# Kernel tuning notes

Hardware: AMD Instinct MI355X
Metric: run time of the kernel (lower is better)

## Reference

```python
import jax, jax.numpy as jnp
import numpy as np

D, H, HD, L, F, V, R, C = 512, 8, 64, 12, 2048, 2048, 1024, 64
B, T, M = 8, 1024, 128


def posenc(t, d):
    pos = jnp.arange(t, dtype=jnp.float32)[:, None]
    div = jnp.exp(jnp.arange(0, d, 2, dtype=jnp.float32) * (-np.log(10000.0) / d))
    pe = jnp.zeros((t, d), jnp.float32)
    pe = pe.at[:, 0::2].set(jnp.sin(pos * div))
    pe = pe.at[:, 1::2].set(jnp.cos(pos * div))
    return pe


def setup_inputs():
    key = jax.random.key(0)
    ks = iter(jax.random.split(key, 32))
    s = 0.02
    x = jax.random.randint(next(ks), (B, T), 1, V)  # avoid padding_idx=0 rows
    chord_positions = jax.random.randint(next(ks), (B, M), 0, T)
    n = lambda shape: jax.random.normal(next(ks), shape, jnp.float32) * s
    emb = n((V, D)).at[0].set(0.0)  # padding_idx row zeroed
    return {
        'x': x, 'chord_positions': chord_positions, 'emb': emb,
        'rel_emb': n((L, 2 * R + 1, HD)),
        'Wq': n((L, D, D)), 'bq': jnp.zeros((L, D)),
        'Wk': n((L, D, D)), 'bk': jnp.zeros((L, D)),
        'Wv': n((L, D, D)), 'bv': jnp.zeros((L, D)),
        'Wo': n((L, D, D)), 'bo': jnp.zeros((L, D)),
        'ln1_s': jnp.ones((L, D)), 'ln1_b': jnp.zeros((L, D)),
        'W1': n((L, D, F)), 'b1': jnp.zeros((L, F)),
        'W2': n((L, F, D)), 'b2': jnp.zeros((L, D)),
        'ln2_s': jnp.ones((L, D)), 'ln2_b': jnp.zeros((L, D)),
        'Wout': n((D, V)), 'bout': jnp.zeros((V,)),
        'Wc': n((D, C)), 'bc': jnp.zeros((C,)),
    }


def _ln(z, s, b):
    mu = jnp.mean(z, -1, keepdims=True)
    var = jnp.var(z, -1, keepdims=True)
    return (z - mu) * jax.lax.rsqrt(var + 1e-5) * s + b


def _forward(x, chord_positions, emb, rel_emb, Wq, bq, Wk, bk, Wv, bv, Wo, bo,
             ln1_s, ln1_b, W1, b1, W2, b2, ln2_s, ln2_b, Wout, bout, Wc, bc):
    Bx, Tx = x.shape
    h = emb[x] * jnp.sqrt(jnp.float32(D)) + posenc(Tx, D)[None]
    pad = (x == 0)  # key padding mask
    causal = jnp.triu(jnp.ones((Tx, Tx), bool), 1)
    mask = causal[None, None] | pad[:, None, None, :]  # (B,1|H,T,T)
    rel_idx = jnp.clip(jnp.arange(Tx)[None, :] - jnp.arange(Tx)[:, None], -R, R) + R  # (T,T)
    for i in range(L):
        q = (h @ Wq[i] + bq[i]).reshape(Bx, Tx, H, HD).transpose(0, 2, 1, 3)
        k = (h @ Wk[i] + bk[i]).reshape(Bx, Tx, H, HD).transpose(0, 2, 1, 3)
        v = (h @ Wv[i] + bv[i]).reshape(Bx, Tx, H, HD).transpose(0, 2, 1, 3)
        scores = jnp.einsum('bhqd,bhkd->bhqk', q, k)
        relp = jnp.einsum('bhqd,rd->bhqr', q, rel_emb[i])  # (B,H,T,2R+1)
        scores = scores + jnp.take_along_axis(relp, rel_idx[None, None], axis=-1)
        scores = scores * (1.0 / np.sqrt(HD))
        scores = jnp.where(mask, -1e9, scores)
        a = jax.nn.softmax(scores, axis=-1)
        o = jnp.einsum('bhqk,bhkd->bhqd', a, v).transpose(0, 2, 1, 3).reshape(Bx, Tx, D)
        h = _ln(h + o @ Wo[i] + bo[i], ln1_s[i], ln1_b[i])
        f = jax.nn.relu(h @ W1[i] + b1[i]) @ W2[i] + b2[i]
        h = _ln(h + f, ln2_s[i], ln2_b[i])
    logits = h @ Wout + bout
    safe_pos = jnp.maximum(chord_positions, 0)
    gathered = h[jnp.arange(Bx)[:, None], safe_pos]  # (B,M,D)
    chord_logits = gathered @ Wc + bc
    return logits, chord_logits


def reference(x, chord_positions, emb, rel_emb, Wq, bq, Wk, bk, Wv, bv, Wo, bo,
              ln1_s, ln1_b, W1, b1, W2, b2, ln2_s, ln2_b, Wout, bout, Wc, bc):
    return _forward(x, chord_positions, emb, rel_emb, Wq, bq, Wk, bk, Wv, bv, Wo, bo,
                    ln1_s, ln1_b, W1, b1, W2, b2, ln2_s, ln2_b, Wout, bout, Wc, bc)
```

## Files before the change

### kernel.cpp

```cpp
#include <hip/hip_runtime.h>
#include <hip/hip_bf16.h>
#include <cstddef>

constexpr int B_ = 8, TT = 1024, H_ = 8, HD_ = 64, D_ = 512, F_ = 2048;
constexpr int L_ = 12, R_ = 1024, NR_ = 2049, C_ = 64, M_ = 128, V_ = 2048;
constexpr int BT_ = B_ * TT;

typedef short bf16x8_t __attribute__((ext_vector_type(8)));
typedef float f32x4_t __attribute__((ext_vector_type(4)));
typedef unsigned short ushort_t;

__device__ __forceinline__ float b2f(unsigned int u16) {
  return __uint_as_float(u16 << 16);
}
__device__ __forceinline__ ushort_t f2b(float f) {
  __hip_bfloat16 h = __float2bfloat16(f);
  return *reinterpret_cast<ushort_t*>(&h);
}

__global__ __launch_bounds__(256) void transpose_bf16_b(const float* __restrict__ src,
                                                        ushort_t* __restrict__ dst,
                                                        int K, int N,
                                                        size_t sstride, size_t dstride) {
  __shared__ float t[32][33];
  src += (size_t)blockIdx.z * sstride;
  dst += (size_t)blockIdx.z * dstride;
  int k0 = blockIdx.y * 32, n0 = blockIdx.x * 32;
  int r = threadIdx.x >> 3, c4 = (threadIdx.x & 7) * 4;
  float4 vv = *(const float4*)(src + (size_t)(k0 + r) * N + n0 + c4);
  t[r][c4] = vv.x; t[r][c4 + 1] = vv.y; t[r][c4 + 2] = vv.z; t[r][c4 + 3] = vv.w;
  __syncthreads();
  ushort4 w;
  w.x = f2b(t[c4 + 0][r]); w.y = f2b(t[c4 + 1][r]);
  w.z = f2b(t[c4 + 2][r]); w.w = f2b(t[c4 + 3][r]);
  *(ushort4*)(dst + (size_t)(n0 + r) * K + k0 + c4) = w;
}

__global__ __launch_bounds__(256) void rel_convert(const float* __restrict__ rel,
                                                   ushort_t* __restrict__ rel_bf) {
  size_t idx = ((size_t)blockIdx.x * 256 + threadIdx.x) * 4;
  const size_t total = (size_t)L_ * NR_ * HD_;
  if (idx >= total) return;
  float4 f = *(const float4*)(rel + idx);
  ushort4 w;
  w.x = f2b(f.x); w.y = f2b(f.y); w.z = f2b(f.z); w.w = f2b(f.w);
  *(ushort4*)(rel_bf + idx) = w;
}

__global__ __launch_bounds__(256) void pack_bias(const float* __restrict__ bq,
                                                 const float* __restrict__ bk,
                                                 const float* __restrict__ bv,
                                                 float* __restrict__ bqkv) {
  int idx = blockIdx.x * 256 + threadIdx.x;
  if (idx >= L_ * 1536) return;
  int l = idx / 1536, c = idx - l * 1536;
  float v;
  if (c < 512) v = bq[l * 512 + c];
  else if (c < 1024) v = bk[l * 512 + (c - 512)];
  else v = bv[l * 512 + (c - 1024)];
  bqkv[idx] = v;
}

__global__ __launch_bounds__(256) void posenc_kernel(float* __restrict__ pe) {
  int t = blockIdx.x;
  int i = threadIdx.x;
  const float c = -9.210340371976184f / 512.0f;
  float div = expf((float)(2 * i) * c);
  float arg = (float)t * div;
  float sv, cv;
  __sincosf(arg, &sv, &cv);
  *(float2*)&pe[(size_t)t * D_ + 2 * i] = make_float2(sv, cv);
}

__global__ __launch_bounds__(256) void embed_kernel(const int* __restrict__ x,
                                                    const float* __restrict__ emb,
                                                    const float* __restrict__ pe,
                                                    float* __restrict__ h,
                                                    ushort_t* __restrict__ h_bf) {
  int bt = blockIdx.x;
  int t = bt & (TT - 1);
  int tok = x[bt];
  size_t base = (size_t)bt * D_;
  size_t ebase = (size_t)tok * D_;
  int d = threadIdx.x * 2;
  float2 e2 = *(const float2*)&emb[ebase + d];
  float2 p2 = *(const float2*)&pe[(size_t)t * D_ + d];
  float v0 = e2.x * 22.627416997969522f + p2.x;
  float v1 = e2.y * 22.627416997969522f + p2.y;
  *(float2*)&h[base + d] = make_float2(v0, v1);
  unsigned int ob = (unsigned int)f2b(v0) | ((unsigned int)f2b(v1) << 16);
  *(unsigned int*)&h_bf[base + d] = ob;
}

template <int OUT_BF16, int RELU>
__global__ __launch_bounds__(256) void gemm_mfma(const ushort_t* __restrict__ A,
                                                 const ushort_t* __restrict__ Bt,
                                                 const float* __restrict__ bias,
                                                 void* __restrict__ Cout,
                                                 int Mm, int N, int K) {
  __shared__ ushort_t As[128 * 32];
  __shared__ ushort_t Bs[128 * 32];
  int tid = threadIdx.x;
  int m0 = blockIdx.y * 128, n0 = blockIdx.x * 128;
  int lane = tid & 63, wid = tid >> 6;
  int wr = wid >> 1, wc = wid & 1;

  f32x4_t acc[4][4];
#pragma unroll
  for (int mi = 0; mi < 4; ++mi)
#pragma unroll
    for (int ni = 0; ni < 4; ++ni) acc[mi][ni] = (f32x4_t){0.f, 0.f, 0.f, 0.f};

  int c0 = tid, c1 = tid + 256;
  int ar0 = c0 >> 2, ap0 = c0 & 3, akg0 = ap0 ^ ((ar0 >> 1) & 3);
  int ar1 = c1 >> 2, ap1 = c1 & 3, akg1 = ap1 ^ ((ar1 >> 1) & 3);
  const ushort_t* Arow0 = A + (size_t)(m0 + ar0) * K + akg0 * 8;
  const ushort_t* Arow1 = A + (size_t)(m0 + ar1) * K + akg1 * 8;
  const ushort_t* Brow0 = Bt + (size_t)(n0 + ar0) * K + akg0 * 8;
  const ushort_t* Brow1 = Bt + (size_t)(n0 + ar1) * K + akg1 * 8;

  uint4 ra0 = *(const uint4*)(Arow0);
  uint4 ra1 = *(const uint4*)(Arow1);
  uint4 rb0 = *(const uint4*)(Brow0);
  uint4 rb1 = *(const uint4*)(Brow1);

  int NT = K >> 5;
  int kg = lane >> 4, rl = lane & 15;
  for (int kt = 0; kt < NT; ++kt) {
    __syncthreads();
    *(uint4*)&As[ar0 * 32 + ap0 * 8] = ra0;
    *(uint4*)&As[ar1 * 32 + ap1 * 8] = ra1;
    *(uint4*)&Bs[ar0 * 32 + ap0 * 8] = rb0;
    *(uint4*)&Bs[ar1 * 32 + ap1 * 8] = rb1;
    __syncthreads();
    if (kt + 1 < NT) {
      int ko = (kt + 1) << 5;
      ra0 = *(const uint4*)(Arow0 + ko);
      ra1 = *(const uint4*)(Arow1 + ko);
      rb0 = *(const uint4*)(Brow0 + ko);
      rb1 = *(const uint4*)(Brow1 + ko);
    }
    bf16x8_t fa[4], fb[4];
#pragma unroll
    for (int mi = 0; mi < 4; ++mi) {
      int r = wr * 64 + mi * 16 + rl;
      fa[mi] = *(bf16x8_t*)&As[r * 32 + ((kg ^ ((r >> 1) & 3)) << 3)];
    }
#pragma unroll
    for (int ni = 0; ni < 4; ++ni) {
      int r = wc * 64 + ni * 16 + rl;
      fb[ni] = *(bf16x8_t*)&Bs[r * 32 + ((kg ^ ((r >> 1) & 3)) << 3)];
    }
#pragma unroll
    for (int mi = 0; mi < 4; ++mi)
#pragma unroll
      for (int ni = 0; ni < 4; ++ni)
        acc[mi][ni] = __builtin_amdgcn_mfma_f32_16x16x32_bf16(fa[mi], fb[ni], acc[mi][ni], 0, 0, 0);
  }

  int rg = lane >> 4;
#pragma unroll
  for (int ni = 0; ni < 4; ++ni) {
    int col = n0 + wc * 64 + ni * 16 + rl;
    float bv = bias[col];
#pragma unroll
    for (int mi = 0; mi < 4; ++mi) {
      int row0 = m0 + wr * 64 + mi * 16 + rg * 4;
#pragma unroll
      for (int r = 0; r < 4; ++r) {
        float vv = acc[mi][ni][r] + bv;
        if (RELU) vv = fmaxf(vv, 0.0f);
        if (OUT_BF16)
          ((ushort_t*)Cout)[(size_t)(row0 + r) * N + col] = f2b(vv);
        else
          ((float*)Cout)[(size_t)(row0 + r) * N + col] = vv;
      }
    }
  }
}

__global__ __launch_bounds__(256) void chord_mfma(const ushort_t* __restrict__ h_bf,
                                                  const int* __restrict__ pos,
                                                  const ushort_t* __restrict__ wcT,
                                                  const float* __restrict__ bc,
                                                  float* __restrict__ out) {
  __shared__ ushort_t As[64 * 32];
  __shared__ ushort_t Bs[64 * 32];
  int tid = threadIdx.x;
  int lane = tid & 63, w = tid >> 6;
  int rl = lane & 15, kg = lane >> 4;
  int m0 = blockIdx.x * 64;
  int ar = tid >> 2, ap = tid & 3, akg = ap ^ ((ar >> 1) & 3);
  int grow = m0 + ar;
  int b = grow >> 7;
  int p = pos[grow];
  if (p < 0) p = 0;
  const ushort_t* asrc = h_bf + ((size_t)(b * TT + p)) * D_ + akg * 8;
  const ushort_t* bsrc = wcT + (size_t)ar * D_ + akg * 8;

  f32x4_t acc[4];
#pragma unroll
  for (int ni = 0; ni < 4; ++ni) acc[ni] = (f32x4_t){0.f, 0.f, 0.f, 0.f};

  for (int kt = 0; kt < 16; ++kt) {
    uint4 va = *(const uint4*)(asrc + kt * 32);
    uint4 vb = *(const uint4*)(bsrc + kt * 32);
    __syncthreads();
    *(uint4*)&As[ar * 32 + ap * 8] = va;
    *(uint4*)&Bs[ar * 32 + ap * 8] = vb;
    __syncthreads();
    int r = 16 * w + rl;
    bf16x8_t fa = *(bf16x8_t*)&As[r * 32 + ((kg ^ ((r >> 1) & 3)) << 3)];
#pragma unroll
    for (int ni = 0; ni < 4; ++ni) {
      int rr = ni * 16 + rl;
      bf16x8_t fb = *(bf16x8_t*)&Bs[rr * 32 + ((kg ^ ((rr >> 1) & 3)) << 3)];
      acc[ni] = __builtin_amdgcn_mfma_f32_16x16x32_bf16(fa, fb, acc[ni], 0, 0, 0);
    }
  }

  int rg = lane >> 4;
#pragma unroll
  for (int ni = 0; ni < 4; ++ni) {
    int col = ni * 16 + rl;
    float bv = bc[col];
#pragma unroll
    for (int r = 0; r < 4; ++r) {
      int row = m0 + 16 * w + rg * 4 + r;
      out[(size_t)row * C_ + col] = acc[ni][r] + bv;
    }
  }
}

__global__ __launch_bounds__(256) void attn_mfma(const ushort_t* __restrict__ qkv,
                                                 const ushort_t* __restrict__ rel_bf,
                                                 ushort_t* __restrict__ o) {
  __shared__ ushort_t QPs[64 * 64];
  __shared__ ushort_t Ks[64 * 64];
  __shared__ ushort_t Vs[64 * 64];
  __shared__ ushort_t Rl[128 * 64];

  int blk = blockIdx.x;
  int u = ((blk & 15) + 5 * ((blk >> 8) & 3)) & 15;
  int qt = (u & 1) ? ((u - 1) >> 1) : (15 - (u >> 1));
  int bh = blk >> 4;
  int hh = bh & 7, b = bh >> 3;
  int t0 = qt << 6;
  int tid = threadIdx.x;
  int lane = tid & 63, w = tid >> 6;
  int lo = lane & 15, hi = lane >> 4;

  const ushort_t* qg = qkv + ((size_t)(b * TT + t0)) * 1536 + hh * 64;
  const ushort_t* kg = qkv + ((size_t)b * TT) * 1536 + 512 + hh * 64;
  const ushort_t* vg = qkv + ((size_t)b * TT) * 1536 + 1024 + hh * 64;
  const ushort_t* relb = rel_bf + (size_t)(961 - t0) * 64;

  int row_a = tid >> 3, gg_a = tid & 7;
  int row_b = row_a + 32;

  for (int idx = tid; idx < 512; idx += 256) {
    int row = idx >> 3, gg = idx & 7;
    uint4 uu = *(const uint4*)(qg + (size_t)row * 1536 + gg * 8);
    unsigned int uw[4] = {uu.x, uu.y, uu.z, uu.w};
    unsigned int ow[4];
#pragma unroll
    for (int j = 0; j < 4; ++j) {
      float f0 = b2f(uw[j] & 0xffffu) * 0.125f;
      float f1 = b2f(uw[j] >> 16) * 0.125f;
      ow[j] = (unsigned int)f2b(f0) | ((unsigned int)f2b(f1) << 16);
    }
    *(uint4*)&QPs[row * 64 + ((gg ^ (row & 7)) << 3)] = make_uint4(ow[0], ow[1], ow[2], ow[3]);
  }
  __syncthreads();

  bf16x8_t faq0 = *(bf16x8_t*)&QPs[(16 * w + lo) * 64 + ((hi ^ (lo & 7)) << 3)];
  bf16x8_t faq1 = *(bf16x8_t*)&QPs[(16 * w + lo) * 64 + (((hi + 4) ^ (lo & 7)) << 3)];

  uint4 pk0 = *(const uint4*)(kg + (size_t)row_a * 1536 + gg_a * 8);
  uint4 pk1 = *(const uint4*)(kg + (size_t)row_b * 1536 + gg_a * 8);
  uint4 pv0 = *(const uint4*)(vg + (size_t)row_a * 1536 + gg_a * 8);
  uint4 pv1 = *(const uint4*)(vg + (size_t)row_b * 1536 + gg_a * 8);
  uint4 pr0 = *(const uint4*)(relb + (size_t)row_a * 64 + gg_a * 8);
  uint4 pr1 = *(const uint4*)(relb + (size_t)(row_a + 32) * 64 + gg_a * 8);
  uint4 pr2 = *(const uint4*)(relb + (size_t)(row_a + 64) * 64 + gg_a * 8);
  uint4 pr3 = *(const uint4*)(relb + (size_t)(row_a + 96) * 64 + gg_a * 8);

  f32x4_t acc_o[4];
#pragma unroll
  for (int nd = 0; nd < 4; ++nd) acc_o[nd] = (f32x4_t){0.f, 0.f, 0.f, 0.f};
  float lrow[4] = {0.f, 0.f, 0.f, 0.f};

  int vsb = (int)(size_t)(const void*)Vs;
  int tb0 = vsb + ((2 * hi + 0) * 4) * 128 + lo * 8;
  int tb1 = vsb + ((2 * hi + 1) * 4) * 128 + lo * 8;
  int tb2 = vsb + ((2 * hi + 8) * 4) * 128 + lo * 8;
  int tb3 = vsb + ((2 * hi + 9) * 4) * 128 + lo * 8;

  int nkt = (t0 >> 6) + 1;
  for (int kt = 0; kt < nkt; ++kt) {
    __syncthreads();
    *(uint4*)&Ks[row_a * 64 + ((gg_a ^ (row_a & 7)) << 3)] = pk0;
    *(uint4*)&Ks[row_b * 64 + ((gg_a ^ (row_b & 7)) << 3)] = pk1;
    *(uint4*)&Vs[((row_a >> 2) * 4 + (gg_a >> 1)) * 64 + (row_a & 3) * 16 + (gg_a & 1) * 8] = pv0;
    *(uint4*)&Vs[((row_b >> 2) * 4 + (gg_a >> 1)) * 64 + (row_b & 3) * 16 + (gg_a & 1) * 8] = pv1;
    if (kt == 0) {
      int u0 = row_a;
      *(uint4*)&Rl[u0 * 64 + ((gg_a ^ (u0 & 7)) << 3)] = pr0;
      int u1 = row_a + 32;
      *(uint4*)&Rl[u1 * 64 + ((gg_a ^ (u1 & 7)) << 3)] = pr1;
      int u2 = row_a + 64;
      *(uint4*)&Rl[u2 * 64 + ((gg_a ^ (u2 & 7)) << 3)] = pr2;
      int u3 = row_a + 96;
      *(uint4*)&Rl[u3 * 64 + ((gg_a ^ (u3 & 7)) << 3)] = pr3;
    } else {
      int ur0 = 64 + row_a, ph0 = (ur0 + (kt << 6)) & 127;
      *(uint4*)&Rl[ph0 * 64 + ((gg_a ^ (ur0 & 7)) << 3)] = pr0;
      int ur1 = 64 + row_b, ph1 = (ur1 + (kt << 6)) & 127;
      *(uint4*)&Rl[ph1 * 64 + ((gg_a ^ (ur1 & 7)) << 3)] = pr1;
    }
    __syncthreads();
    if (kt + 1 < nkt) {
      size_t ko = (size_t)((kt + 1) << 6);
      pk0 = *(const uint4*)(kg + (ko + row_a) * 1536 + gg_a * 8);
      pk1 = *(const uint4*)(kg + (ko + row_b) * 1536 + gg_a * 8);
      pv0 = *(const uint4*)(vg + (ko + row_a) * 1536 + gg_a * 8);
      pv1 = *(const uint4*)(vg + (ko + row_b) * 1536 + gg_a * 8);
      pr0 = *(const uint4*)(relb + (ko + 64 + row_a) * 64 + gg_a * 8);
      pr1 = *(const uint4*)(relb + (ko + 64 + row_b) * 64 + gg_a * 8);
    }

    f32x4_t acc_s[4], acc_r[5];
#pragma unroll
    for (int nc = 0; nc < 4; ++nc) acc_s[nc] = (f32x4_t){0.f, 0.f, 0.f, 0.f};
#pragma unroll
    for (int pt = 0; pt < 5; ++pt) acc_r[pt] = (f32x4_t){0.f, 0.f, 0.f, 0.f};

    __builtin_amdgcn_s_setprio(1);
#pragma unroll
    for (int nc = 0; nc < 4; ++nc) {
      int row = 16 * nc + lo;
      bf16x8_t fb0 = *(bf16x8_t*)&Ks[row * 64 + ((hi ^ (lo & 7)) << 3)];
      bf16x8_t fb1 = *(bf16x8_t*)&Ks[row * 64 + (((hi + 4) ^ (lo & 7)) << 3)];
      acc_s[nc] = __builtin_amdgcn_mfma_f32_16x16x32_bf16(faq0, fb0, acc_s[nc], 0, 0, 0);
      acc_s[nc] = __builtin_amdgcn_mfma_f32_16x16x32_bf16(faq1, fb1, acc_s[nc], 0, 0, 0);
    }
#pragma unroll
    for (int pt = 0; pt < 5; ++pt) {
      int r = 16 * (3 - w + pt) + lo;
      int phys = (r + (kt << 6)) & 127;
      bf16x8_t fb0 = *(bf16x8_t*)&Rl[phys * 64 + ((hi ^ (lo & 7)) << 3)];
      bf16x8_t fb1 = *(bf16x8_t*)&Rl[phys * 64 + (((hi + 4) ^ (lo & 7)) << 3)];
      acc_r[pt] = __builtin_amdgcn_mfma_f32_16x16x32_bf16(faq0, fb0, acc_r[pt], 0, 0, 0);
      acc_r[pt] = __builtin_amdgcn_mfma_f32_16x16x32_bf16(faq1, fb1, acc_r[pt], 0, 0, 0);
    }
    __builtin_amdgcn_s_setprio(0);

    bool islast = (kt == nkt - 1);
#pragma unroll
    for (int g = 0; g < 4; ++g) {
      int rl = 4 * hi + g;
      int dd = lo + 15 - rl;
      int src = (lane & 48) | (dd & 15);
      bool carry = (dd & 16) != 0;
      float sh0 = __shfl(acc_r[0][g], src);
      float sh1 = __shfl(acc_r[1][g], src);
      float sh2 = __shfl(acc_r[2][g], src);
      float sh3 = __shfl(acc_r[3][g], src);
      float sh4 = __shfl(acc_r[4][g], src);
      float s0 = acc_s[0][g] + (carry ? sh1 : sh0);
      float s1 = acc_s[1][g] + (carry ? sh2 : sh1);
      float s2 = acc_s[2][g] + (carry ? sh3 : sh2);
      float s3 = acc_s[3][g] + (carry ? sh4 : sh3);
      if (islast) {
        int rw = 16 * w + rl;
        if (lo > rw) s0 = -1e30f;
        if (16 + lo > rw) s1 = -1e30f;
        if (32 + lo > rw) s2 = -1e30f;
        if (48 + lo > rw) s3 = -1e30f;
      }
      float p0 = __expf(s0);
      float p1 = __expf(s1);
      float p2 = __expf(s2);
      float p3 = __expf(s3);
      float ls = p0 + p1 + p2 + p3;
      ls += __shfl_xor(ls, 1);
      ls += __shfl_xor(ls, 2);
      ls += __shfl_xor(ls, 4);
      ls += __shfl_xor(ls, 8);
      lrow[g] += ls;
      ushort_t* pr = &QPs[(16 * w + rl) * 64];
      int rsw = rl & 7, l3 = lo >> 3, l7 = lo & 7;
      pr[(((0 + l3) ^ rsw) << 3) + l7] = f2b(p0);
      pr[(((2 + l3) ^ rsw) << 3) + l7] = f2b(p1);
      pr[(((4 + l3) ^ rsw) << 3) + l7] = f2b(p2);
      pr[(((6 + l3) ^ rsw) << 3) + l7] = f2b(p3);
    }

    bf16x8_t pa0 = *(bf16x8_t*)&QPs[(16 * w + lo) * 64 + ((hi ^ (lo & 7)) << 3)];
    bf16x8_t pa1 = *(bf16x8_t*)&QPs[(16 * w + lo) * 64 + (((hi + 4) ^ (lo & 7)) << 3)];
    unsigned long long tr0[4], tr1[4], tr2[4], tr3[4];
#pragma unroll
    for (int nd = 0; nd < 4; ++nd) {
      asm volatile("ds_read_b64_tr_b16 %0, %1" : "=v"(tr0[nd]) : "v"(tb0 + nd * 128));
      asm volatile("ds_read_b64_tr_b16 %0, %1" : "=v"(tr1[nd]) : "v"(tb1 + nd * 128));
      asm volatile("ds_read_b64_tr_b16 %0, %1" : "=v"(tr2[nd]) : "v"(tb2 + nd * 128));
      asm volatile("ds_read_b64_tr_b16 %0, %1" : "=v"(tr3[nd]) : "v"(tb3 + nd * 128));
    }
    asm volatile("s_waitcnt lgkmcnt(0)" ::: "memory");
    __builtin_amdgcn_sched_barrier(0);
    __builtin_amdgcn_s_setprio(1);
#pragma unroll
    for (int nd = 0; nd < 4; ++nd) {
      union { unsigned long long u[2]; bf16x8_t v; } cv0, cv1;
      cv0.u[0] = tr0[nd]; cv0.u[1] = tr1[nd];
      cv1.u[0] = tr2[nd]; cv1.u[1] = tr3[nd];
      acc_o[nd] = __builtin_amdgcn_mfma_f32_16x16x32_bf16(pa0, cv0.v, acc_o[nd], 0, 0, 0);
      acc_o[nd] = __builtin_amdgcn_mfma_f32_16x16x32_bf16(pa1, cv1.v, acc_o[nd], 0, 0, 0);
    }
    __builtin_amdgcn_s_setprio(0);
  }

  ushort_t* og = o + ((size_t)(b * TT + t0 + 16 * w)) * D_ + hh * HD_;
#pragma unroll
  for (int g = 0; g < 4; ++g) {
    int rl = 4 * hi + g;
    float inv = 1.0f / lrow[g];
#pragma unroll
    for (int nd = 0; nd < 4; ++nd)
      og[(size_t)rl * D_ + 16 * nd + lo] = f2b(acc_o[nd][g] * inv);
  }
}

__global__ __launch_bounds__(256) void ln_res_kernel(float* __restrict__ h,
                                                     const ushort_t* __restrict__ y_bf,
                                                     const float* __restrict__ s,
                                                     const float* __restrict__ bvec,
                                                     ushort_t* __restrict__ h_bf) {
  int w = threadIdx.x >> 6, lane = threadIdx.x & 63;
  int row = blockIdx.x * 4 + w;
  size_t base = (size_t)row * D_ + lane * 8;
  float4 h0 = *(const float4*)&h[base];
  float4 h1 = *(const float4*)&h[base + 4];
  uint4 yy = *(const uint4*)&y_bf[base];
  float z[8];
  z[0] = h0.x + b2f(yy.x & 0xffffu); z[1] = h0.y + b2f(yy.x >> 16);
  z[2] = h0.z + b2f(yy.y & 0xffffu); z[3] = h0.w + b2f(yy.y >> 16);
  z[4] = h1.x + b2f(yy.z & 0xffffu); z[5] = h1.y + b2f(yy.z >> 16);
  z[6] = h1.z + b2f(yy.w & 0xffffu); z[7] = h1.w + b2f(yy.w >> 16);
  float s1 = 0.f, s2 = 0.f;
#pragma unroll
  for (int j = 0; j < 8; ++j) {
    s1 += z[j];
    s2 += z[j] * z[j];
  }
#pragma unroll
  for (int off = 1; off < 64; off <<= 1) {
    s1 += __shfl_xor(s1, off);
    s2 += __shfl_xor(s2, off);
  }
  float mu = s1 * (1.0f / 512.0f);
  float var = s2 * (1.0f / 512.0f) - mu * mu;
  float rs = rsqrtf(var + 1e-5f);
  int d = lane * 8;
  float4 sc0 = *(const float4*)&s[d];
  float4 sc1 = *(const float4*)&s[d + 4];
  float4 bb0 = *(const float4*)&bvec[d];
  float4 bb1 = *(const float4*)&bvec[d + 4];
  float o_[8];
  o_[0] = (z[0] - mu) * rs * sc0.x + bb0.x; o_[1] = (z[1] - mu) * rs * sc0.y + bb0.y;
  o_[2] = (z[2] - mu) * rs * sc0.z + bb0.z; o_[3] = (z[3] - mu) * rs * sc0.w + bb0.w;
  o_[4] = (z[4] - mu) * rs * sc1.x + bb1.x; o_[5] = (z[5] - mu) * rs * sc1.y + bb1.y;
  o_[6] = (z[6] - mu) * rs * sc1.z + bb1.z; o_[7] = (z[7] - mu) * rs * sc1.w + bb1.w;
  *(float4*)&h[base] = make_float4(o_[0], o_[1], o_[2], o_[3]);
  *(float4*)&h[base + 4] = make_float4(o_[4], o_[5], o_[6], o_[7]);
  uint4 ob;
  ob.x = (unsigned int)f2b(o_[0]) | ((unsigned int)f2b(o_[1]) << 16);
  ob.y = (unsigned int)f2b(o_[2]) | ((unsigned int)f2b(o_[3]) << 16);
  ob.z = (unsigned int)f2b(o_[4]) | ((unsigned int)f2b(o_[5]) << 16);
  ob.w = (unsigned int)f2b(o_[6]) | ((unsigned int)f2b(o_[7]) << 16);
  *(uint4*)&h_bf[base] = ob;
}

extern "C" void kernel_launch(void* const* d_in, const int* in_sizes, int n_in,
                              void* d_out, int out_size, void* d_ws, size_t ws_size,
                              hipStream_t stream) {
  const int* x = (const int*)d_in[0];
  const int* cpos = (const int*)d_in[1];
  const float* emb = (const float*)d_in[2];
  const float* rel = (const float*)d_in[3];
  const float* Wq = (const float*)d_in[4];
  const float* bq = (const float*)d_in[5];
  const float* Wk = (const float*)d_in[6];
  const float* bk = (const float*)d_in[7];
  const float* Wv = (const float*)d_in[8];
  const float* bv = (const float*)d_in[9];
  const float* Wo = (const float*)d_in[10];
  const float* bo = (const float*)d_in[11];
  const float* ln1s = (const float*)d_in[12];
  const float* ln1b = (const float*)d_in[13];
  const float* W1 = (const float*)d_in[14];
  const float* b1 = (const float*)d_in[15];
  const float* W2 = (const float*)d_in[16];
  const float* b2 = (const float*)d_in[17];
  const float* ln2s = (const float*)d_in[18];
  const float* ln2b = (const float*)d_in[19];
  const float* Wout = (const float*)d_in[20];
  const float* bout = (const float*)d_in[21];
  const float* Wc = (const float*)d_in[22];
  const float* bc = (const float*)d_in[23];

  const size_t SZ = (size_t)BT_ * D_;
  const size_t WPROJ = (size_t)D_ * D_;
  const size_t WFFN = (size_t)D_ * F_;

  float* h = (float*)d_ws;
  ushort_t* y_bf = (ushort_t*)(h + SZ);
  ushort_t* h_bf = (ushort_t*)(h + 2 * SZ);
  ushort_t* qkv_bf = h_bf + SZ;
  ushort_t* o_bf = qkv_bf + (size_t)BT_ * 1536;
  ushort_t* mid_bf = o_bf + SZ;
  ushort_t* wqkvT = mid_bf + (size_t)BT_ * F_;
  ushort_t* woT = wqkvT + (size_t)L_ * 1536 * 512;
  ushort_t* w1T = woT + L_ * WPROJ;
  ushort_t* w2T = w1T + L_ * WFFN;
  ushort_t* woutT = w2T + L_ * WFFN;
  ushort_t* wcT = woutT + (size_t)D_ * V_;
  ushort_t* rel_bf = wcT + (size_t)D_ * C_;
  float* bqkv = (float*)(rel_bf + (size_t)L_ * NR_ * HD_);
  float* pe = bqkv + L_ * 1536;
  float* out = (float*)d_out;

  transpose_bf16_b<<<dim3(16, 16, 12), 256, 0, stream>>>(Wq, wqkvT, 512, 512, WPROJ, (size_t)1536 * 512);
  transpose_bf16_b<<<dim3(16, 16, 12), 256, 0, stream>>>(Wk, wqkvT + (size_t)512 * 512, 512, 512, WPROJ, (size_t)1536 * 512);
  transpose_bf16_b<<<dim3(16, 16, 12), 256, 0, stream>>>(Wv, wqkvT + (size_t)1024 * 512, 512, 512, WPROJ, (size_t)1536 * 512);
  transpose_bf16_b<<<dim3(16, 16, 12), 256, 0, stream>>>(Wo, woT, 512, 512, WPROJ, WPROJ);
  transpose_bf16_b<<<dim3(64, 16, 12), 256, 0, stream>>>(W1, w1T, 512, 2048, WFFN, WFFN);
  transpose_bf16_b<<<dim3(16, 64, 12), 256, 0, stream>>>(W2, w2T, 2048, 512, WFFN, WFFN);
  transpose_bf16_b<<<dim3(64, 16, 1), 256, 0, stream>>>(Wout, woutT, 512, 2048, 0, 0);
  transpose_bf16_b<<<dim3(2, 16, 1), 256, 0, stream>>>(Wc, wcT, 512, 64, 0, 0);
  rel_convert<<<1537, 256, 0, stream>>>(rel, rel_bf);
  pack_bias<<<(L_ * 1536 + 255) / 256, 256, 0, stream>>>(bq, bk, bv, bqkv);
  posenc_kernel<<<TT, 256, 0, stream>>>(pe);

  embed_kernel<<<BT_, 256, 0, stream>>>(x, emb, pe, h, h_bf);

  dim3 gQKV(1536 / 128, BT_ / 128);
  dim3 gProj(D_ / 128, BT_ / 128);
  dim3 gF1(F_ / 128, BT_ / 128);
  dim3 gOut(V_ / 128, BT_ / 128);

  for (int l = 0; l < L_; ++l) {
    gemm_mfma<1, 0><<<gQKV, 256, 0, stream>>>(h_bf, wqkvT + (size_t)l * 1536 * 512,
                                              bqkv + l * 1536, qkv_bf, BT_, 1536, D_);
    attn_mfma<<<B_ * H_ * (TT / 64), 256, 0, stream>>>(qkv_bf, rel_bf + (size_t)l * NR_ * HD_, o_bf);
    gemm_mfma<1, 0><<<gProj, 256, 0, stream>>>(o_bf, woT + l * WPROJ, bo + l * D_, y_bf, BT_, D_, D_);
    ln_res_kernel<<<BT_ / 4, 256, 0, stream>>>(h, y_bf, ln1s + l * D_, ln1b + l * D_, h_bf);
    gemm_mfma<1, 1><<<gF1, 256, 0, stream>>>(h_bf, w1T + l * WFFN, b1 + l * F_, mid_bf, BT_, F_, D_);
    gemm_mfma<1, 0><<<gProj, 256, 0, stream>>>(mid_bf, w2T + l * WFFN, b2 + l * D_, y_bf, BT_, D_, F_);
    ln_res_kernel<<<BT_ / 4, 256, 0, stream>>>(h, y_bf, ln2s + l * D_, ln2b + l * D_, h_bf);
  }

  gemm_mfma<0, 0><<<gOut, 256, 0, stream>>>(h_bf, woutT, bout, out, BT_, V_, D_);
  chord_mfma<<<(B_ * M_) / 64, 256, 0, stream>>>(h_bf, cpos, wcT, bc, out + (size_t)BT_ * V_);
}
```

Measured before the change: 2.202 ms.

## Split attention key tiles across two wave groups with cross-group reduction

The attention kernel now runs 512 threads per block. Two groups of four waves each process alternating 64-key tiles for the same 64-query tile, using separate K/V shared buffers and a wider 192-row relative-embedding window. At the end, the second group's partial outputs and row sums go through shared memory and are added by the first group before normalisation. This is meant to halve the serial key-loop length per block and raise occupancy on the causal tiles. The cost is more shared memory, a reduction step, and idle waves on odd tile counts.

```diff
diff --git a/kernel.cpp b/kernel.cpp
--- a/kernel.cpp
+++ b/kernel.cpp
@@ -232,13 +232,13 @@
   }
 }
 
-__global__ __launch_bounds__(256) void attn_mfma(const ushort_t* __restrict__ qkv,
+__global__ __launch_bounds__(512) void attn_mfma(const ushort_t* __restrict__ qkv,
                                                  const ushort_t* __restrict__ rel_bf,
                                                  ushort_t* __restrict__ o) {
-  __shared__ ushort_t QPs[64 * 64];
-  __shared__ ushort_t Ks[64 * 64];
-  __shared__ ushort_t Vs[64 * 64];
-  __shared__ ushort_t Rl[128 * 64];
+  __shared__ ushort_t QPs[128 * 64];
+  __shared__ ushort_t Ks[2][64 * 64];
+  __shared__ ushort_t Vs[2][64 * 64];
+  __shared__ ushort_t Rl[192 * 64];
 
   int blk = blockIdx.x;
   int u = ((blk & 15) + 5 * ((blk >> 8) & 3)) & 15;
@@ -249,17 +249,19 @@
   int tid = threadIdx.x;
   int lane = tid & 63, w = tid >> 6;
   int lo = lane & 15, hi = lane >> 4;
+  int wg = w & 3, g4 = w >> 2;
 
   const ushort_t* qg = qkv + ((size_t)(b * TT + t0)) * 1536 + hh * 64;
   const ushort_t* kg = qkv + ((size_t)b * TT) * 1536 + 512 + hh * 64;
   const ushort_t* vg = qkv + ((size_t)b * TT) * 1536 + 1024 + hh * 64;
   const ushort_t* relb = rel_bf + (size_t)(961 - t0) * 64;
 
-  int row_a = tid >> 3, gg_a = tid & 7;
+  int g_tid = tid & 255;
+  int row_a = g_tid >> 3, gg_a = g_tid & 7;
   int row_b = row_a + 32;
 
-  for (int idx = tid; idx < 512; idx += 256) {
-    int row = idx >> 3, gg = idx & 7;
+  {
+    int row = tid >> 3, gg = tid & 7;
     uint4 uu = *(const uint4*)(qg + (size_t)row * 1536 + gg * 8);
     unsigned int uw[4] = {uu.x, uu.y, uu.z, uu.w};
     unsigned int ow[4];
@@ -273,161 +275,183 @@
   }
   __syncthreads();
 
-  bf16x8_t faq0 = *(bf16x8_t*)&QPs[(16 * w + lo) * 64 + ((hi ^ (lo & 7)) << 3)];
-  bf16x8_t faq1 = *(bf16x8_t*)&QPs[(16 * w + lo) * 64 + (((hi + 4) ^ (lo & 7)) << 3)];
-
-  uint4 pk0 = *(const uint4*)(kg + (size_t)row_a * 1536 + gg_a * 8);
-  uint4 pk1 = *(const uint4*)(kg + (size_t)row_b * 1536 + gg_a * 8);
-  uint4 pv0 = *(const uint4*)(vg + (size_t)row_a * 1536 + gg_a * 8);
-  uint4 pv1 = *(const uint4*)(vg + (size_t)row_b * 1536 + gg_a * 8);
-  uint4 pr0 = *(const uint4*)(relb + (size_t)row_a * 64 + gg_a * 8);
-  uint4 pr1 = *(const uint4*)(relb + (size_t)(row_a + 32) * 64 + gg_a * 8);
-  uint4 pr2 = *(const uint4*)(relb + (size_t)(row_a + 64) * 64 + gg_a * 8);
-  uint4 pr3 = *(const uint4*)(relb + (size_t)(row_a + 96) * 64 + gg_a * 8);
+  bf16x8_t faq0 = *(bf16x8_t*)&QPs[(16 * wg + lo) * 64 + ((hi ^ (lo & 7)) << 3)];
+  bf16x8_t faq1 = *(bf16x8_t*)&QPs[(16 * wg + lo) * 64 + (((hi + 4) ^ (lo & 7)) << 3)];
+
+  int nkt = qt + 1;
+  int nIt = (nkt + 1) >> 1;
+
+  {
+  }
+  int k00 = g4 << 6;
+  uint4 pk0 = *(const uint4*)(kg + (size_t)(k00 + row_a) * 1536 + gg_a * 8);
+  uint4 pk1 = *(const uint4*)(kg + (size_t)(k00 + row_b) * 1536 + gg_a * 8);
+  uint4 pv0 = *(const uint4*)(vg + (size_t)(k00 + row_a) * 1536 + gg_a * 8);
+  uint4 pv1 = *(const uint4*)(vg + (size_t)(k00 + row_b) * 1536 + gg_a * 8);
+  int ur0 = tid >> 3, gg_r = tid & 7;
+  uint4 pr0 = *(const uint4*)(relb + (size_t)ur0 * 64 + gg_r * 8);
+  uint4 pr1 = *(const uint4*)(relb + (size_t)(ur0 + 64) * 64 + gg_r * 8);
+  uint4 pr2 = *(const uint4*)(relb + (size_t)(ur0 + 128) * 64 + gg_r * 8);
 
   f32x4_t acc_o[4];
 #pragma unroll
   for (int nd = 0; nd < 4; ++nd) acc_o[nd] = (f32x4_t){0.f, 0.f, 0.f, 0.f};
   float lrow[4] = {0.f, 0.f, 0.f, 0.f};
 
-  int vsb = (int)(size_t)(const void*)Vs;
+  int vsb = (int)(size_t)(const void*)&Vs[g4][0];
   int tb0 = vsb + ((2 * hi + 0) * 4) * 128 + lo * 8;
   int tb1 = vsb + ((2 * hi + 1) * 4) * 128 + lo * 8;
   int tb2 = vsb + ((2 * hi + 8) * 4) * 128 + lo * 8;
   int tb3 = vsb + ((2 * hi + 9) * 4) * 128 + lo * 8;
 
-  int nkt = (t0 >> 6) + 1;
-  for (int kt = 0; kt < nkt; ++kt) {
+  for (int it = 0; it < nIt; ++it) {
+    int kti = 2 * it + g4;
+    bool active = kti < nkt;
     __syncthreads();
-    *(uint4*)&Ks[row_a * 64 + ((gg_a ^ (row_a & 7)) << 3)] = pk0;
-    *(uint4*)&Ks[row_b * 64 + ((gg_a ^ (row_b & 7)) << 3)] = pk1;
-    *(uint4*)&Vs[((row_a >> 2) * 4 + (gg_a >> 1)) * 64 + (row_a & 3) * 16 + (gg_a & 1) * 8] = pv0;
-    *(uint4*)&Vs[((row_b >> 2) * 4 + (gg_a >> 1)) * 64 + (row_b & 3) * 16 + (gg_a & 1) * 8] = pv1;
-    if (kt == 0) {
-      int u0 = row_a;
-      *(uint4*)&Rl[u0 * 64 + ((gg_a ^ (u0 & 7)) << 3)] = pr0;
-      int u1 = row_a + 32;
-      *(uint4*)&Rl[u1 * 64 + ((gg_a ^ (u1 & 7)) << 3)] = pr1;
-      int u2 = row_a + 64;
-      *(uint4*)&Rl[u2 * 64 + ((gg_a ^ (u2 & 7)) << 3)] = pr2;
-      int u3 = row_a + 96;
-      *(uint4*)&Rl[u3 * 64 + ((gg_a ^ (u3 & 7)) << 3)] = pr3;
-    } else {
-      int ur0 = 64 + row_a, ph0 = (ur0 + (kt << 6)) & 127;
-      *(uint4*)&Rl[ph0 * 64 + ((gg_a ^ (ur0 & 7)) << 3)] = pr0;
-      int ur1 = 64 + row_b, ph1 = (ur1 + (kt << 6)) & 127;
-      *(uint4*)&Rl[ph1 * 64 + ((gg_a ^ (ur1 & 7)) << 3)] = pr1;
+    *(uint4*)&Ks[g4][row_a * 64 + ((gg_a ^ (row_a & 7)) << 3)] = pk0;
+    *(uint4*)&Ks[g4][row_b * 64 + ((gg_a ^ (row_b & 7)) << 3)] = pk1;
+    *(uint4*)&Vs[g4][((row_a >> 2) * 4 + (gg_a >> 1)) * 64 + (row_a & 3) * 16 + (gg_a & 1) * 8] = pv0;
+    *(uint4*)&Vs[g4][((row_b >> 2) * 4 + (gg_a >> 1)) * 64 + (row_b & 3) * 16 + (gg_a & 1) * 8] = pv1;
+    {
+      int r0 = ur0, r1 = ur0 + 64, r2 = ur0 + 128;
+      int sw = (ur0 & 7) << 3;
+      *(uint4*)&Rl[r0 * 64 + (gg_r << 3 ^ sw)] = pr0;
+      *(uint4*)&Rl[r1 * 64 + (gg_r << 3 ^ sw)] = pr1;
+      *(uint4*)&Rl[r2 * 64 + (gg_r << 3 ^ sw)] = pr2;
     }
     __syncthreads();
-    if (kt + 1 < nkt) {
-      size_t ko = (size_t)((kt + 1) << 6);
-      pk0 = *(const uint4*)(kg + (ko + row_a) * 1536 + gg_a * 8);
-      pk1 = *(const uint4*)(kg + (ko + row_b) * 1536 + gg_a * 8);
-      pv0 = *(const uint4*)(vg + (ko + row_a) * 1536 + gg_a * 8);
-      pv1 = *(const uint4*)(vg + (ko + row_b) * 1536 + gg_a * 8);
-      pr0 = *(const uint4*)(relb + (ko + 64 + row_a) * 64 + gg_a * 8);
-      pr1 = *(const uint4*)(relb + (ko + 64 + row_b) * 64 + gg_a * 8);
-    }
-
-    f32x4_t acc_s[4], acc_r[5];
-#pragma unroll
-    for (int nc = 0; nc < 4; ++nc) acc_s[nc] = (f32x4_t){0.f, 0.f, 0.f, 0.f};
-#pragma unroll
-    for (int pt = 0; pt < 5; ++pt) acc_r[pt] = (f32x4_t){0.f, 0.f, 0.f, 0.f};
-
-    __builtin_amdgcn_s_setprio(1);
-#pragma unroll
-    for (int nc = 0; nc < 4; ++nc) {
-      int row = 16 * nc + lo;
-      bf16x8_t fb0 = *(bf16x8_t*)&Ks[row * 64 + ((hi ^ (lo & 7)) << 3)];
-      bf16x8_t fb1 = *(bf16x8_t*)&Ks[row * 64 + (((hi + 4) ^ (lo & 7)) << 3)];
-      acc_s[nc] = __builtin_amdgcn_mfma_f32_16x16x32_bf16(faq0, fb0, acc_s[nc], 0, 0, 0);
-      acc_s[nc] = __builtin_amdgcn_mfma_f32_16x16x32_bf16(faq1, fb1, acc_s[nc], 0, 0, 0);
-    }
-#pragma unroll
-    for (int pt = 0; pt < 5; ++pt) {
-      int r = 16 * (3 - w + pt) + lo;
-      int phys = (r + (kt << 6)) & 127;
-      bf16x8_t fb0 = *(bf16x8_t*)&Rl[phys * 64 + ((hi ^ (lo & 7)) << 3)];
-      bf16x8_t fb1 = *(bf16x8_t*)&Rl[phys * 64 + (((hi + 4) ^ (lo & 7)) << 3)];
-      acc_r[pt] = __builtin_amdgcn_mfma_f32_16x16x32_bf16(faq0, fb0, acc_r[pt], 0, 0, 0);
-      acc_r[pt] = __builtin_amdgcn_mfma_f32_16x16x32_bf16(faq1, fb1, acc_r[pt], 0, 0, 0);
-    }
-    __builtin_amdgcn_s_setprio(0);
-
-    bool islast = (kt == nkt - 1);
+    if (it + 1 < nIt) {
+      int k0n = (2 * (it + 1) + g4) << 6;
+      if (k0n > TT - 64) k0n = TT - 64;
+      pk0 = *(const uint4*)(kg + (size_t)(k0n + row_a) * 1536 + gg_a * 8);
+      pk1 = *(const uint4*)(kg + (size_t)(k0n + row_b) * 1536 + gg_a * 8);
+      pv0 = *(const uint4*)(vg + (size_t)(k0n + row_a) * 1536 + gg_a * 8);
+      pv1 = *(const uint4*)(vg + (size_t)(k0n + row_b) * 1536 + gg_a * 8);
+      size_t wb = (size_t)(128 * (it + 1));
+      pr0 = *(const uint4*)(relb + (wb + ur0) * 64 + gg_r * 8);
+      pr1 = *(const uint4*)(relb + (wb + ur0 + 64) * 64 + gg_r * 8);
+      pr2 = *(const uint4*)(relb + (wb + ur0 + 128) * 64 + gg_r * 8);
+    }
+
+    if (active) {
+      f32x4_t acc_s[4], acc_r[5];
+#pragma unroll
+      for (int nc = 0; nc < 4; ++nc) acc_s[nc] = (f32x4_t){0.f, 0.f, 0.f, 0.f};
+#pragma unroll
+      for (int pt = 0; pt < 5; ++pt) acc_r[pt] = (f32x4_t){0.f, 0.f, 0.f, 0.f};
+
+      __builtin_amdgcn_s_setprio(1);
+#pragma unroll
+      for (int nc = 0; nc < 4; ++nc) {
+        int row = 16 * nc + lo;
+        bf16x8_t fb0 = *(bf16x8_t*)&Ks[g4][row * 64 + ((hi ^ (lo & 7)) << 3)];
+        bf16x8_t fb1 = *(bf16x8_t*)&Ks[g4][row * 64 + (((hi + 4) ^ (lo & 7)) << 3)];
+        acc_s[nc] = __builtin_amdgcn_mfma_f32_16x16x32_bf16(faq0, fb0, acc_s[nc], 0, 0, 0);
+        acc_s[nc] = __builtin_amdgcn_mfma_f32_16x16x32_bf16(faq1, fb1, acc_s[nc], 0, 0, 0);
+      }
+#pragma unroll
+      for (int pt = 0; pt < 5; ++pt) {
+        int r = 64 * g4 + 16 * (3 - wg + pt) + lo;
+        bf16x8_t fb0 = *(bf16x8_t*)&Rl[r * 64 + ((hi ^ (lo & 7)) << 3)];
+        bf16x8_t fb1 = *(bf16x8_t*)&Rl[r * 64 + (((hi + 4) ^ (lo & 7)) << 3)];
+        acc_r[pt] = __builtin_amdgcn_mfma_f32_16x16x32_bf16(faq0, fb0, acc_r[pt], 0, 0, 0);
+        acc_r[pt] = __builtin_amdgcn_mfma_f32_16x16x32_bf16(faq1, fb1, acc_r[pt], 0, 0, 0);
+      }
+      __builtin_amdgcn_s_setprio(0);
+
+      bool islast = (kti == nkt - 1);
+#pragma unroll
+      for (int g = 0; g < 4; ++g) {
+        int rl = 4 * hi + g;
+        int dd = lo + 15 - rl;
+        int src = (lane & 48) | (dd & 15);
+        bool carry = (dd & 16) != 0;
+        float sh0 = __shfl(acc_r[0][g], src);
+        float sh1 = __shfl(acc_r[1][g], src);
+        float sh2 = __shfl(acc_r[2][g], src);
+        float sh3 = __shfl(acc_r[3][g], src);
+        float sh4 = __shfl(acc_r[4][g], src);
+        float s0 = acc_s[0][g] + (carry ? sh1 : sh0);
+        float s1 = acc_s[1][g] + (carry ? sh2 : sh1);
+        float s2 = acc_s[2][g] + (carry ? sh3 : sh2);
+        float s3 = acc_s[3][g] + (carry ? sh4 : sh3);
+        if (islast) {
+          int rw = 16 * wg + rl;
+          if (lo > rw) s0 = -1e30f;
+          if (16 + lo > rw) s1 = -1e30f;
+          if (32 + lo > rw) s2 = -1e30f;
+          if (48 + lo > rw) s3 = -1e30f;
+        }
+        float p0 = __expf(s0);
+        float p1 = __expf(s1);
+        float p2 = __expf(s2);
+        float p3 = __expf(s3);
+        float ls = p0 + p1 + p2 + p3;
+        ls += __shfl_xor(ls, 1);
+        ls += __shfl_xor(ls, 2);
+        ls += __shfl_xor(ls, 4);
+        ls += __shfl_xor(ls, 8);
+        lrow[g] += ls;
+        ushort_t* pr = &QPs[(16 * w + rl) * 64];
+        int rsw = rl & 7, l3 = lo >> 3, l7 = lo & 7;
+        pr[(((0 + l3) ^ rsw) << 3) + l7] = f2b(p0);
+        pr[(((2 + l3) ^ rsw) << 3) + l7] = f2b(p1);
+        pr[(((4 + l3) ^ rsw) << 3) + l7] = f2b(p2);
+        pr[(((6 + l3) ^ rsw) << 3) + l7] = f2b(p3);
+      }
+
+      bf16x8_t pa0 = *(bf16x8_t*)&QPs[(16 * w + lo) * 64 + ((hi ^ (lo & 7)) << 3)];
+      bf16x8_t pa1 = *(bf16x8_t*)&QPs[(16 * w + lo) * 64 + (((hi + 4) ^ (lo & 7)) << 3)];
+      unsigned long long tr0[4], tr1[4], tr2[4], tr3[4];
+#pragma unroll
+      for (int nd = 0; nd < 4; ++nd) {
+        asm volatile("ds_read_b64_tr_b16 %0, %1" : "=v"(tr0[nd]) : "v"(tb0 + nd * 128));
+        asm volatile("ds_read_b64_tr_b16 %0, %1" : "=v"(tr1[nd]) : "v"(tb1 + nd * 128));
+        asm volatile("ds_read_b64_tr_b16 %0, %1" : "=v"(tr2[nd]) : "v"(tb2 + nd * 128));
+        asm volatile("ds_read_b64_tr_b16 %0, %1" : "=v"(tr3[nd]) : "v"(tb3 + nd * 128));
+      }
+      asm volatile("s_waitcnt lgkmcnt(0)" ::: "memory");
+      __builtin_amdgcn_sched_barrier(0);
+      __builtin_amdgcn_s_setprio(1);
+#pragma unroll
+      for (int nd = 0; nd < 4; ++nd) {
+        union { unsigned long long u[2]; bf16x8_t v; } cv0, cv1;
+        cv0.u[0] = tr0[nd]; cv0.u[1] = tr1[nd];
+        cv1.u[0] = tr2[nd]; cv1.u[1] = tr3[nd];
+        acc_o[nd] = __builtin_amdgcn_mfma_f32_16x16x32_bf16(pa0, cv0.v, acc_o[nd], 0, 0, 0);
+        acc_o[nd] = __builtin_amdgcn_mfma_f32_16x16x32_bf16(pa1, cv1.v, acc_o[nd], 0, 0, 0);
+      }
+      __builtin_amdgcn_s_setprio(0);
+    }
+  }
+
+  __syncthreads();
+  float* sO = (float*)Rl;
+  float* sL = sO + 4 * 16 * 64;
+  if (g4 == 1) {
 #pragma unroll
     for (int g = 0; g < 4; ++g) {
       int rl = 4 * hi + g;
-      int dd = lo + 15 - rl;
-      int src = (lane & 48) | (dd & 15);
-      bool carry = (dd & 16) != 0;
-      float sh0 = __shfl(acc_r[0][g], src);
-      float sh1 = __shfl(acc_r[1][g], src);
-      float sh2 = __shfl(acc_r[2][g], src);
-      float sh3 = __shfl(acc_r[3][g], src);
-      float sh4 = __shfl(acc_r[4][g], src);
-      float s0 = acc_s[0][g] + (carry ? sh1 : sh0);
-      float s1 = acc_s[1][g] + (carry ? sh2 : sh1);
-      float s2 = acc_s[2][g] + (carry ? sh3 : sh2);
-      float s3 = acc_s[3][g] + (carry ? sh4 : sh3);
-      if (islast) {
-        int rw = 16 * w + rl;
-        if (lo > rw) s0 = -1e30f;
-        if (16 + lo > rw) s1 = -1e30f;
-        if (32 + lo > rw) s2 = -1e30f;
-        if (48 + lo > rw) s3 = -1e30f;
-      }
-      float p0 = __expf(s0);
-      float p1 = __expf(s1);
-      float p2 = __expf(s2);
-      float p3 = __expf(s3);
-      float ls = p0 + p1 + p2 + p3;
-      ls += __shfl_xor(ls, 1);
-      ls += __shfl_xor(ls, 2);
-      ls += __shfl_xor(ls, 4);
-      ls += __shfl_xor(ls, 8);
-      lrow[g] += ls;
-      ushort_t* pr = &QPs[(16 * w + rl) * 64];
-      int rsw = rl & 7, l3 = lo >> 3, l7 = lo & 7;
-      pr[(((0 + l3) ^ rsw) << 3) + l7] = f2b(p0);
-      pr[(((2 + l3) ^ rsw) << 3) + l7] = f2b(p1);
-      pr[(((4 + l3) ^ rsw) << 3) + l7] = f2b(p2);
-      pr[(((6 + l3) ^ rsw) << 3) + l7] = f2b(p3);
-    }
-
-    bf16x8_t pa0 = *(bf16x8_t*)&QPs[(16 * w + lo) * 64 + ((hi ^ (lo & 7)) << 3)];
-    bf16x8_t pa1 = *(bf16x8_t*)&QPs[(16 * w + lo) * 64 + (((hi + 4) ^ (lo & 7)) << 3)];
-    unsigned long long tr0[4], tr1[4], tr2[4], tr3[4];
-#pragma unroll
-    for (int nd = 0; nd < 4; ++nd) {
-      asm volatile("ds_read_b64_tr_b16 %0, %1" : "=v"(tr0[nd]) : "v"(tb0 + nd * 128));
-      asm volatile("ds_read_b64_tr_b16 %0, %1" : "=v"(tr1[nd]) : "v"(tb1 + nd * 128));
-      asm volatile("ds_read_b64_tr_b16 %0, %1" : "=v"(tr2[nd]) : "v"(tb2 + nd * 128));
-      asm volatile("ds_read_b64_tr_b16 %0, %1" : "=v"(tr3[nd]) : "v"(tb3 + nd * 128));
-    }
-    asm volatile("s_waitcnt lgkmcnt(0)" ::: "memory");
-    __builtin_amdgcn_sched_barrier(0);
-    __builtin_amdgcn_s_setprio(1);
-#pragma unroll
-    for (int nd = 0; nd < 4; ++nd) {
-      union { unsigned long long u[2]; bf16x8_t v; } cv0, cv1;
-      cv0.u[0] = tr0[nd]; cv0.u[1] = tr1[nd];
-      cv1.u[0] = tr2[nd]; cv1.u[1] = tr3[nd];
-      acc_o[nd] = __builtin_amdgcn_mfma_f32_16x16x32_bf16(pa0, cv0.v, acc_o[nd], 0, 0, 0);
-      acc_o[nd] = __builtin_amdgcn_mfma_f32_16x16x32_bf16(pa1, cv1.v, acc_o[nd], 0, 0, 0);
-    }
-    __builtin_amdgcn_s_setprio(0);
-  }
-
-  ushort_t* og = o + ((size_t)(b * TT + t0 + 16 * w)) * D_ + hh * HD_;
-#pragma unroll
-  for (int g = 0; g < 4; ++g) {
-    int rl = 4 * hi + g;
-    float inv = 1.0f / lrow[g];
-#pragma unroll
-    for (int nd = 0; nd < 4; ++nd)
-      og[(size_t)rl * D_ + 16 * nd + lo] = f2b(acc_o[nd][g] * inv);
+#pragma unroll
+      for (int nd = 0; nd < 4; ++nd)
+        sO[(wg * 16 + rl) * 64 + 16 * nd + lo] = acc_o[nd][g];
+      if (lo == 0) sL[wg * 16 + rl] = lrow[g];
+    }
+  }
+  __syncthreads();
+  if (g4 == 0) {
+    ushort_t* og = o + ((size_t)(b * TT + t0 + 16 * wg)) * D_ + hh * HD_;
+#pragma unroll
+    for (int g = 0; g < 4; ++g) {
+      int rl = 4 * hi + g;
+      float lsum = lrow[g] + sL[wg * 16 + rl];
+      float inv = 1.0f / lsum;
+#pragma unroll
+      for (int nd = 0; nd < 4; ++nd) {
+        float ov = acc_o[nd][g] + sO[(wg * 16 + rl) * 64 + 16 * nd + lo];
+        og[(size_t)rl * D_ + 16 * nd + lo] = f2b(ov * inv);
+      }
+    }
   }
 }
 
@@ -552,7 +576,7 @@
   for (int l = 0; l < L_; ++l) {
     gemm_mfma<1, 0><<<gQKV, 256, 0, stream>>>(h_bf, wqkvT + (size_t)l * 1536 * 512,
                                               bqkv + l * 1536, qkv_bf, BT_, 1536, D_);
-    attn_mfma<<<B_ * H_ * (TT / 64), 256, 0, stream>>>(qkv_bf, rel_bf + (size_t)l * NR_ * HD_, o_bf);
+    attn_mfma<<<B_ * H_ * 16, 512, 0, stream>>>(qkv_bf, rel_bf + (size_t)l * NR_ * HD_, o_bf);
     gemm_mfma<1, 0><<<gProj, 256, 0, stream>>>(o_bf, woT + l * WPROJ, bo + l * D_, y_bf, BT_, D_, D_);
     ln_res_kernel<<<BT_ / 4, 256, 0, stream>>>(h, y_bf, ln1s + l * D_, ln1b + l * D_, h_bf);
     gemm_mfma<1, 1><<<gF1, 256, 0, stream>>>(h_bf, w1T + l * WFFN, b1 + l * F_, mid_bf, BT_, F_, D_);
```

Result: slower. 2.303 ms (+4.6%).
